# Kernel tuning notes

Hardware: AMD Instinct MI355X
Metric: run time of the kernel (lower is better)

## Reference

```python
import jax, jax.numpy as jnp
import numpy as np


def setup_inputs() -> dict:
    key = jax.random.key(0)
    B, N, F = 32, 8192, 256
    x = jax.random.normal(key, (B, N, F), dtype=jnp.float32)
    return {"x": x, "k": 1024}


def reference(x, k):
    # Sort rows of each graph by last feature, descending, keep top k.
    # Original: per-batch argsort(desc) + gather, then truncate to k (N > k here).
    # lax.top_k returns indices of the k largest values in descending order,
    # equivalent to argsort(desc)[:k] without a full sort.
    _, idx = jax.lax.top_k(x[..., -1], k)          # idx: [B, k]
    out = jnp.take_along_axis(x, idx[:, :, None], axis=1)  # [B, k, F]
    return out
```

## Files before the change

kernel.cpp:

```cpp
#include <hip/hip_runtime.h>
#include <hip/hip_bf16.h>

#define B_DIM 32
#define N_DIM 8192
#define F_DIM 256
#define K_DIM 1024
#define RUNS_PER_B 8

__device__ __forceinline__ unsigned int f32_ord(float v) {
    unsigned int u = __float_as_uint(v);
    return (u & 0x80000000u) ? ~u : (u | 0x80000000u);
}

__global__ __launch_bounds__(512)
void sort_runs_kernel(const float* __restrict__ x,
                      unsigned long long* __restrict__ runs) {
    __shared__ unsigned long long K[K_DIM];

    const int blk = blockIdx.x;
    const int b   = blk >> 3;
    const int c   = blk & 7;
    const float* xcol = x + (size_t)b * N_DIM * F_DIM + (F_DIM - 1);
    const int base = c * K_DIM;

    for (int i = threadIdx.x; i < K_DIM; i += 512) {
        int row = base + i;
        float v = xcol[(size_t)row * F_DIM];
        K[i] = ((unsigned long long)f32_ord(v) << 32) |
               (unsigned int)(N_DIM - 1 - row);
    }
    __syncthreads();

    for (unsigned int kk = 2; kk <= K_DIM; kk <<= 1) {
        for (unsigned int jj = kk >> 1; jj > 0; jj >>= 1) {
            unsigned int p = threadIdx.x;
            unsigned int i = ((p & ~(jj - 1)) << 1) | (p & (jj - 1));
            unsigned int j = i | jj;
            unsigned long long a  = K[i];
            unsigned long long bb = K[j];
            bool desc = ((i & kk) == 0);
            if (desc ? (a < bb) : (a > bb)) { K[i] = bb; K[j] = a; }
            __syncthreads();
        }
    }

    ulonglong2* dst = (ulonglong2*)(runs + (size_t)blk * K_DIM);
    const ulonglong2* src = (const ulonglong2*)K;
    dst[threadIdx.x] = src[threadIdx.x];
}

__global__ __launch_bounds__(1024)
void merge_topk_kernel(const unsigned long long* __restrict__ runs,
                       int* __restrict__ idx_out) {
    __shared__ unsigned long long K[N_DIM];

    const int b = blockIdx.x;
    const ulonglong2* src = (const ulonglong2*)(runs + (size_t)b * N_DIM);
    ulonglong2* Kv = (ulonglong2*)K;
    for (unsigned int i = threadIdx.x; i < N_DIM / 2; i += 1024) Kv[i] = src[i];
    __syncthreads();

    for (int level = 0; level < 3; ++level) {
        const unsigned int m      = 4u >> level;
        const unsigned int stride = 1024u << level;
        const unsigned int shift  = 11 + level;

        for (unsigned int t = threadIdx.x; t < m * 1024u; t += 1024) {
            unsigned int g = t >> 10, i = t & 1023u;
            unsigned int a = g << shift;
            unsigned long long bv = K[a + stride + 1023u - i];
            if (bv > K[a + i]) K[a + i] = bv;
        }
        __syncthreads();

        for (unsigned int jj = 512; jj > 0; jj >>= 1) {
            for (unsigned int t = threadIdx.x; t < m * 512u; t += 1024) {
                unsigned int g = t >> 9, p = t & 511u;
                unsigned int base = g << shift;
                unsigned int i = base + (((p & ~(jj - 1)) << 1) | (p & (jj - 1)));
                unsigned int j = i | jj;
                unsigned long long a = K[i];
                unsigned long long c = K[j];
                if (a < c) { K[i] = c; K[j] = a; }
            }
            __syncthreads();
        }
    }

    for (unsigned int i = threadIdx.x; i < K_DIM; i += 1024) {
        unsigned int low = (unsigned int)(K[i] & 0xFFFFFFFFu);
        idx_out[b * K_DIM + i] = (int)(N_DIM - 1 - low);
    }
}

__global__ __launch_bounds__(256)
void gather_rows_kernel(const float* __restrict__ x,
                        const int* __restrict__ idx,
                        float* __restrict__ out) {
    size_t gid = (size_t)blockIdx.x * blockDim.x + threadIdx.x;
    int f4     = (int)(gid & (F_DIM / 4 - 1));
    size_t row = gid >> 6;
    int b      = (int)(row >> 10);
    int src    = idx[row];

    const float4* src_ptr =
        (const float4*)(x + ((size_t)b * N_DIM + (size_t)src) * F_DIM) + f4;
    ((float4*)out)[gid] = *src_ptr;
}

extern "C" void kernel_launch(void* const* d_in, const int* in_sizes, int n_in,
                              void* d_out, int out_size, void* d_ws, size_t ws_size,
                              hipStream_t stream) {
    const float* x = (const float*)d_in[0];
    float* out = (float*)d_out;

    unsigned long long* runs = (unsigned long long*)d_ws;
    int* idx_ws = (int*)((char*)d_ws + (size_t)B_DIM * N_DIM * 8);

    sort_runs_kernel<<<B_DIM * RUNS_PER_B, 512, 0, stream>>>(x, runs);
    merge_topk_kernel<<<B_DIM, 1024, 0, stream>>>(runs, idx_ws);

    const size_t total_f4 = (size_t)B_DIM * K_DIM * F_DIM / 4;
    gather_rows_kernel<<<(int)(total_f4 / 256), 256, 0, stream>>>(x, idx_ws, out);
}
```

Before: 344.2 us.

## Replace sort-and-merge top-k with histogram radix select plus small bitonic sort

Two kernels, one sorting 1024-element runs and one merging them, are replaced by a single per-batch kernel. It builds a 13-bit histogram of the keys, finds the threshold bin by prefix scan, collects candidates above that bin, and ranks the tie bin by brute force. Only the selected 1024 keys are then bitonic-sorted. This removes the runs workspace round trip and one launch, and cuts sort work from 8192 to 1024 elements. In exchange, parallelism drops to 32 blocks, and a threshold bin with more than 1024 entries would be truncated.

New measurement: 353.6 us. 2.7% more time.

```diff
diff --git a/kernel.cpp b/kernel.cpp
--- a/kernel.cpp
+++ b/kernel.cpp
@@ -1,96 +1,124 @@
 #include <hip/hip_runtime.h>
-#include <hip/hip_bf16.h>
 
 #define B_DIM 32
 #define N_DIM 8192
 #define F_DIM 256
 #define K_DIM 1024
-#define RUNS_PER_B 8
+
+#define NBITS 13
+#define NBINS (1 << NBITS)
+#define BPT   (NBINS / 1024)
+#define KPT   (N_DIM / 1024)
+#define TCAP  1024
 
 __device__ __forceinline__ unsigned int f32_ord(float v) {
     unsigned int u = __float_as_uint(v);
     return (u & 0x80000000u) ? ~u : (u | 0x80000000u);
 }
 
-__global__ __launch_bounds__(512)
-void sort_runs_kernel(const float* __restrict__ x,
-                      unsigned long long* __restrict__ runs) {
-    __shared__ unsigned long long K[K_DIM];
+__global__ __launch_bounds__(1024)
+void select_sort_kernel(const float* __restrict__ x, int* __restrict__ idx_out) {
+    __shared__ unsigned int       HIST[NBINS];
+    __shared__ unsigned int       P[1024];
+    __shared__ unsigned long long SEL[K_DIM];
+    __shared__ unsigned long long L[TCAP];
+    __shared__ unsigned int       sc[4];
 
-    const int blk = blockIdx.x;
-    const int b   = blk >> 3;
-    const int c   = blk & 7;
+    const int b = blockIdx.x;
+    const int t = threadIdx.x;
     const float* xcol = x + (size_t)b * N_DIM * F_DIM + (F_DIM - 1);
-    const int base = c * K_DIM;
 
-    for (int i = threadIdx.x; i < K_DIM; i += 512) {
-        int row = base + i;
+    #pragma unroll
+    for (int i = 0; i < BPT; ++i) HIST[t + i * 1024] = 0;
+    if (t < 4) sc[t] = 0;
+
+    unsigned long long key[KPT];
+    #pragma unroll
+    for (int i = 0; i < KPT; ++i) {
+        int row = t + i * 1024;
         float v = xcol[(size_t)row * F_DIM];
-        K[i] = ((unsigned long long)f32_ord(v) << 32) |
-               (unsigned int)(N_DIM - 1 - row);
+        key[i] = ((unsigned long long)f32_ord(v) << 32) |
+                 (unsigned int)(N_DIM - 1 - row);
+    }
+    __syncthreads();
+
+    #pragma unroll
+    for (int i = 0; i < KPT; ++i)
+        atomicAdd(&HIST[(unsigned int)(key[i] >> (64 - NBITS))], 1u);
+    __syncthreads();
+
+    {
+        unsigned int s = 0;
+        #pragma unroll
+        for (int i = 0; i < BPT; ++i) s += HIST[t * BPT + i];
+        P[t] = s;
+        __syncthreads();
+        for (int off = 1; off < 1024; off <<= 1) {
+            unsigned int v = P[t] + ((t + off < 1024) ? P[t + off] : 0u);
+            __syncthreads();
+            P[t] = v;
+            __syncthreads();
+        }
+    }
+
+    if (P[t] >= K_DIM && (t == 1023 || P[t + 1] < K_DIM)) sc[2] = (unsigned int)t;
+    __syncthreads();
+    if (t == 0) {
+        unsigned int g   = sc[2];
+        unsigned int run = (g == 1023) ? 0u : P[g + 1];
+        unsigned int T = 0, C1 = 0;
+        for (int bin = (int)g * BPT + BPT - 1; bin >= (int)g * BPT; --bin) {
+            unsigned int c = HIST[bin];
+            if (run + c >= K_DIM) { T = (unsigned int)bin; C1 = run; break; }
+            run += c;
+        }
+        sc[2] = T; sc[3] = C1;
+    }
+    __syncthreads();
+
+    const unsigned int T  = sc[2];
+    const unsigned int C1 = sc[3];
+    const unsigned int R  = K_DIM - C1;
+
+    #pragma unroll
+    for (int i = 0; i < KPT; ++i) {
+        unsigned int bin = (unsigned int)(key[i] >> (64 - NBITS));
+        if (bin > T) {
+            SEL[atomicAdd(&sc[0], 1u)] = key[i];
+        } else if (bin == T) {
+            unsigned int pos = atomicAdd(&sc[1], 1u);
+            if (pos < TCAP) L[pos] = key[i];
+        }
+    }
+    __syncthreads();
+
+    const unsigned int nT = min(sc[1], (unsigned int)TCAP);
+    for (unsigned int i = t; i < nT; i += 1024) {
+        unsigned long long kv = L[i];
+        unsigned int rank = 0;
+        for (unsigned int j = 0; j < nT; ++j) rank += (L[j] > kv) ? 1u : 0u;
+        if (rank < R) SEL[C1 + rank] = kv;
     }
     __syncthreads();
 
     for (unsigned int kk = 2; kk <= K_DIM; kk <<= 1) {
         for (unsigned int jj = kk >> 1; jj > 0; jj >>= 1) {
-            unsigned int p = threadIdx.x;
-            unsigned int i = ((p & ~(jj - 1)) << 1) | (p & (jj - 1));
-            unsigned int j = i | jj;
-            unsigned long long a  = K[i];
-            unsigned long long bb = K[j];
-            bool desc = ((i & kk) == 0);
-            if (desc ? (a < bb) : (a > bb)) { K[i] = bb; K[j] = a; }
-            __syncthreads();
-        }
-    }
-
-    ulonglong2* dst = (ulonglong2*)(runs + (size_t)blk * K_DIM);
-    const ulonglong2* src = (const ulonglong2*)K;
-    dst[threadIdx.x] = src[threadIdx.x];
-}
-
-__global__ __launch_bounds__(1024)
-void merge_topk_kernel(const unsigned long long* __restrict__ runs,
-                       int* __restrict__ idx_out) {
-    __shared__ unsigned long long K[N_DIM];
-
-    const int b = blockIdx.x;
-    const ulonglong2* src = (const ulonglong2*)(runs + (size_t)b * N_DIM);
-    ulonglong2* Kv = (ulonglong2*)K;
-    for (unsigned int i = threadIdx.x; i < N_DIM / 2; i += 1024) Kv[i] = src[i];
-    __syncthreads();
-
-    for (int level = 0; level < 3; ++level) {
-        const unsigned int m      = 4u >> level;
-        const unsigned int stride = 1024u << level;
-        const unsigned int shift  = 11 + level;
-
-        for (unsigned int t = threadIdx.x; t < m * 1024u; t += 1024) {
-            unsigned int g = t >> 10, i = t & 1023u;
-            unsigned int a = g << shift;
-            unsigned long long bv = K[a + stride + 1023u - i];
-            if (bv > K[a + i]) K[a + i] = bv;
-        }
-        __syncthreads();
-
-        for (unsigned int jj = 512; jj > 0; jj >>= 1) {
-            for (unsigned int t = threadIdx.x; t < m * 512u; t += 1024) {
-                unsigned int g = t >> 9, p = t & 511u;
-                unsigned int base = g << shift;
-                unsigned int i = base + (((p & ~(jj - 1)) << 1) | (p & (jj - 1)));
+            if (t < 512) {
+                unsigned int p = (unsigned int)t;
+                unsigned int i = ((p & ~(jj - 1)) << 1) | (p & (jj - 1));
                 unsigned int j = i | jj;
-                unsigned long long a = K[i];
-                unsigned long long c = K[j];
-                if (a < c) { K[i] = c; K[j] = a; }
+                unsigned long long a = SEL[i];
+                unsigned long long c = SEL[j];
+                bool desc = ((i & kk) == 0);
+                if (desc ? (a < c) : (a > c)) { SEL[i] = c; SEL[j] = a; }
             }
             __syncthreads();
         }
     }
 
-    for (unsigned int i = threadIdx.x; i < K_DIM; i += 1024) {
-        unsigned int low = (unsigned int)(K[i] & 0xFFFFFFFFu);
-        idx_out[b * K_DIM + i] = (int)(N_DIM - 1 - low);
-    }
+    for (unsigned int i = t; i < K_DIM; i += 1024)
+        idx_out[b * K_DIM + i] =
+            (int)(N_DIM - 1 - (unsigned int)(SEL[i] & 0xFFFFFFFFu));
 }
 
 __global__ __launch_bounds__(256)
@@ -114,11 +142,9 @@
     const float* x = (const float*)d_in[0];
     float* out = (float*)d_out;
 
-    unsigned long long* runs = (unsigned long long*)d_ws;
-    int* idx_ws = (int*)((char*)d_ws + (size_t)B_DIM * N_DIM * 8);
+    int* idx_ws = (int*)d_ws;
 
-    sort_runs_kernel<<<B_DIM * RUNS_PER_B, 512, 0, stream>>>(x, runs);
-    merge_topk_kernel<<<B_DIM, 1024, 0, stream>>>(runs, idx_ws);
+    select_sort_kernel<<<B_DIM, 1024, 0, stream>>>(x, idx_ws);
 
     const size_t total_f4 = (size_t)B_DIM * K_DIM * F_DIM / 4;
     gather_rows_kernel<<<(int)(total_f4 / 256), 256, 0, stream>>>(x, idx_ws, out);
```
